# Optimization experiments

Measured on AMD Instinct MI355X. Metric: run time of the kernel, lower is better.

## Reference

```python
import jax, jax.numpy as jnp
import numpy as np

UP = 2
KSIZE = 3
RES = 64
LRELU_SLOPE = 0.2
ACT_GAIN = float(np.sqrt(2.0))  # def_gain of 'lrelu' in bias_act


def _setup_filter():
    # upfirdn2d.setup_filter([1,3,3,1]): normalize, make separable 2D filter
    f = jnp.array([1.0, 3.0, 3.0, 1.0], dtype=jnp.float32)
    f = f / jnp.sum(f)
    return jnp.outer(f, f)  # [4,4]


def _upfirdn2d_up2(x, f2):
    # Zero-insertion upsample by 2 + pad + FIR filter, gain = up**2.
    # Torch path: zero-insert to 2H, pad (3,2), conv 4-tap -> 2H+2.
    # lhs_dilation gives 2H-1; absorbing the trailing inserted zero into the
    # right pad ((3,3) instead of (3,2)) is exactly equivalent.
    B, C, H, W = x.shape
    k = (f2 * (UP * UP)).astype(x.dtype)[None, None]  # [1,1,4,4] (symmetric, flip-invariant)
    k = jnp.tile(k, (C, 1, 1, 1))                     # depthwise [C,1,4,4]
    return jax.lax.conv_general_dilated(
        x, k, window_strides=(1, 1), padding=((3, 3), (3, 3)),
        lhs_dilation=(UP, UP),
        dimension_numbers=('NCHW', 'OIHW', 'NCHW'),
        feature_group_count=C)


def setup_inputs() -> dict:
    key = jax.random.key(0)
    ks = jax.random.split(key, 6)
    B, Cin, Cout, Wd = 16, 512, 512, 512
    Hin = RES // UP
    return {
        "x": jax.random.normal(ks[0], (B, Cin, Hin, Hin), jnp.float32),
        "w": jax.random.normal(ks[1], (B, Wd), jnp.float32),
        "affine_weight": jax.random.normal(ks[2], (Cin, Wd), jnp.float32),
        "affine_bias": jnp.ones((Cin,), jnp.float32),  # bias_init=1
        "weight": jax.random.normal(ks[3], (Cout, Cin, KSIZE, KSIZE), jnp.float32),
        "bias": jnp.zeros((Cout,), jnp.float32),
        "noise_const": jax.random.normal(ks[4], (RES, RES), jnp.float32),
        "noise_strength": jax.random.uniform(ks[5], (), jnp.float32),
    }


def reference(x, w, affine_weight, affine_bias, weight, bias, noise_const, noise_strength):
    B, Cin, Hin, Win = x.shape
    Cout = weight.shape[0]
    # affine: FullyConnectedLayer, weight_gain = 1/sqrt(w_dim), bias_init=1
    styles = w @ affine_weight.T * (1.0 / np.sqrt(w.shape[1])) + affine_bias  # [B,Cin]
    # modulate + demodulate (fused_modconv=True): per-sample weights
    wmod = weight[None] * styles[:, None, :, None, None]                     # [B,Cout,Cin,kh,kw]
    dcoef = jax.lax.rsqrt(jnp.sum(jnp.square(wmod), axis=(2, 3, 4)) + 1e-8)  # [B,Cout]
    wmod = wmod * dcoef[:, :, None, None, None]
    # up=2 -> flip_weight=False -> true convolution: flip spatial taps
    wmod = wmod[..., ::-1, ::-1]
    # conv2d_resample: upfirdn2d upsample first (pad = k//2 + (fw+up-1)//2 = 3), then VALID conv
    xu = _upfirdn2d_up2(x, _setup_filter())                                  # [B,Cin,66,66]
    xr = xu.reshape(1, B * Cin, xu.shape[2], xu.shape[3])
    wr = wmod.reshape(B * Cout, Cin, KSIZE, KSIZE)
    y = jax.lax.conv_general_dilated(
        xr, wr, window_strides=(1, 1), padding='VALID',
        dimension_numbers=('NCHW', 'OIHW', 'NCHW'),
        feature_group_count=B)
    y = y.reshape(B, Cout, RES, RES)
    # noise_mode='const': noise = noise_const * noise_strength
    y = y + noise_const * noise_strength
    # fused bias + lrelu + def_gain (gain=1, conv_clamp=None)
    y = jax.nn.leaky_relu(y + bias[None, :, None, None], LRELU_SLOPE) * ACT_GAIN
    return y
```

## Files before the change

kernel.cpp:

```cpp
#include <hip/hip_runtime.h>
#include <hip/hip_bf16.h>
#include <math.h>

#define CIN   512
#define COUT  512
#define NB    16
#define WD    512
#define HIN   32
#define RES   64
#define LRELU 0.2f
#define ACT_GAIN 1.4142135623730951f

typedef __attribute__((ext_vector_type(8))) short short8;
typedef __attribute__((ext_vector_type(4))) float float4v;
typedef __attribute__((ext_vector_type(16))) float float16v;

__global__ void styles2_kernel(const float* __restrict__ w,
                               const float* __restrict__ aw,
                               const float* __restrict__ ab,
                               float* __restrict__ styles) {
    int b = blockIdx.x;
    int cig = blockIdx.y;
    int lane = threadIdx.x & 63, wv = threadIdx.x >> 6;
    __shared__ float wsh[WD];
    for (int e = threadIdx.x; e < WD; e += 256) wsh[e] = w[b * WD + e];
    __syncthreads();
    for (int r = 0; r < 16; ++r) {
        int ci = cig * 64 + wv * 16 + r;
        const float* arow = aw + (size_t)ci * WD;
        float acc = 0.f;
        for (int k = lane; k < WD; k += 64) acc += arow[k] * wsh[k];
        for (int off = 32; off; off >>= 1) acc += __shfl_down(acc, off, 64);
        if (lane == 0)
            styles[b * CIN + ci] = acc * 0.04419417382415922f + ab[ci];
    }
}

__global__ void prep_weights(const float* __restrict__ weight,
                             float* __restrict__ wsq,
                             __hip_bfloat16* __restrict__ gb) {
    int gid = blockIdx.x * 256 + threadIdx.x;
    int co = gid & 511;
    int cig = gid >> 9;
    int cc = cig >> 2, chi = cig & 3;
    int cib = cc * 32 + chi * 8;
    int cog = co >> 5, colo = co & 31;

    float wv[8][3][3];
#pragma unroll
    for (int clo = 0; clo < 8; ++clo) {
        const float* wp = weight + ((size_t)co * CIN + cib + clo) * 9;
        float s = 0.f;
#pragma unroll
        for (int ay = 0; ay < 3; ++ay)
#pragma unroll
            for (int ax = 0; ax < 3; ++ax) {
                float v = wp[ay * 3 + ax];
                wv[clo][ay][ax] = v;
                s += v * v;
            }
        wsq[(size_t)co * CIN + cib + clo] = s;
    }

    const float cr[2][3][3] = {
        {{0.f, 0.25f, 0.75f}, {0.75f, 0.75f, 0.25f}, {0.25f, 0.f, 0.f}},
        {{0.f, 0.f, 0.25f},  {0.25f, 0.75f, 0.75f}, {0.75f, 0.25f, 0.f}}};

#pragma unroll
    for (int phy = 0; phy < 2; ++phy) {
        float tmp[8][3][3];
#pragma unroll
        for (int clo = 0; clo < 8; ++clo)
#pragma unroll
            for (int dy = 0; dy < 3; ++dy)
#pragma unroll
                for (int ax = 0; ax < 3; ++ax)
                    tmp[clo][dy][ax] = cr[phy][dy][0] * wv[clo][0][ax]
                                     + cr[phy][dy][1] * wv[clo][1][ax]
                                     + cr[phy][dy][2] * wv[clo][2][ax];
#pragma unroll
        for (int phx = 0; phx < 2; ++phx) {
            int n = phx * 32 + colo;
#pragma unroll
            for (int dy = 0; dy < 3; ++dy)
#pragma unroll
                for (int dx = 0; dx < 3; ++dx) {
                    int t = dy * 3 + dx;
                    short8 sv;
#pragma unroll
                    for (int clo = 0; clo < 8; ++clo) {
                        float g = tmp[clo][dy][0] * cr[phx][dx][0]
                                + tmp[clo][dy][1] * cr[phx][dx][1]
                                + tmp[clo][dy][2] * cr[phx][dx][2];
                        __hip_bfloat16 h = __float2bfloat16(g);
                        sv[clo] = *reinterpret_cast<const short*>(&h);
                    }
                    size_t off = ((((((size_t)cc * 2 + phy) * 9 + t) * 4 + chi)
                                   * 16 + cog) * 64 + n) * 8;
                    *reinterpret_cast<short8*>(gb + off) = sv;
                }
        }
    }
}

__global__ void dcoef2_kernel(const float* __restrict__ styles,
                              const float* __restrict__ wsq,
                              float* __restrict__ dcoef) {
    int b = blockIdx.x;
    int cog = blockIdx.y;
    int lane = threadIdx.x & 63, wv = threadIdx.x >> 6;
    __shared__ float s2[CIN];
    for (int e = threadIdx.x; e < CIN; e += 256) {
        float s = styles[b * CIN + e];
        s2[e] = s * s;
    }
    __syncthreads();
    for (int r = 0; r < 16; ++r) {
        int co = cog * 64 + wv * 16 + r;
        const float* qrow = wsq + (size_t)co * CIN;
        float acc = 0.f;
        for (int k = lane; k < CIN; k += 64) acc += qrow[k] * s2[k];
        for (int off = 32; off; off >>= 1) acc += __shfl_down(acc, off, 64);
        if (lane == 0) dcoef[b * COUT + co] = rsqrtf(acc + 1e-8f);
    }
}

__global__ void xmod_kernel(const float* __restrict__ x,
                            const float* __restrict__ styles,
                            __hip_bfloat16* __restrict__ xb) {
    __shared__ float xt[128 * 36];
    __shared__ float ssh[128];
    const int r = blockIdx.x;
    const int ci0 = blockIdx.y * 128;
    const int b = blockIdx.z;
    if (threadIdx.x < 128) ssh[threadIdx.x] = styles[b * CIN + ci0 + threadIdx.x];
    const bool inr = (r >= 1) && (r <= 32);
    if (inr) {
        for (int e = threadIdx.x; e < 1024; e += 256) {
            int ci = e >> 3, iw4 = e & 7;
            float4v v = *(const float4v*)(
                x + ((size_t)(b * CIN + ci0 + ci) * HIN + (r - 1)) * HIN + iw4 * 4);
            *(float4v*)(&xt[ci * 36 + iw4 * 4]) = v;
        }
    }
    __syncthreads();
    for (int e = threadIdx.x; e < 544; e += 256) {
        int c = e >> 4, t16 = e & 15;
        short8 sv;
#pragma unroll
        for (int u = 0; u < 8; ++u) {
            int ci = t16 * 8 + u;
            float val = 0.f;
            if (inr && c >= 1 && c <= 32) val = xt[ci * 36 + (c - 1)] * ssh[ci];
            __hip_bfloat16 h = __float2bfloat16(val);
            sv[u] = *reinterpret_cast<const short*>(&h);
        }
        *reinterpret_cast<short8*>(
            xb + (((size_t)b * 34 + r) * 34 + c) * CIN + ci0 + t16 * 8) = sv;
    }
}

#define ABUF 39936
#define BBUF 36864
#define BUFSZ (ABUF + BBUF)
#define LDS_TOT (2 * BUFSZ)

__global__ __launch_bounds__(512, 1) void conv_mfma(
        const __hip_bfloat16* __restrict__ xb,
        const __hip_bfloat16* __restrict__ gb,
        const float* __restrict__ dcoef,
        const float* __restrict__ bias,
        const float* __restrict__ noise,
        const float* __restrict__ nstr,
        float* __restrict__ out)
{
    extern __shared__ __align__(16) char smem[];
    const int tid = threadIdx.x;
    const int lane = tid & 63;
    const int wid = tid >> 6;
    const int li32 = lane & 31;
    const int hi = lane >> 5;
    const int mb = blockIdx.x;
    const int cog = blockIdx.y;
    const int bz = blockIdx.z;
    const int b  = bz >> 1;
    const int phy = bz & 1;
    const int y0 = mb * 16;

    int a_goff[5];
#pragma unroll
    for (int k = 0; k < 5; ++k) {
        int n = wid + k * 8;
        int s = n * 64 + lane;
        if (s > 2447) s = 2447;
        int cr = s / 136;
        int rem = s - cr * 136;
        int chi = rem / 34;
        int col = rem - chi * 34;
        a_goff[k] = (((b * 34 + y0 + cr) * 34 + col)) * CIN + chi * 8;
    }
    int b_goff[5];
#pragma unroll
    for (int k = 0; k < 5; ++k) {
        int sl = wid + k * 8;
        b_goff[k] = phy * 589824 + (sl * 16 + cog) * 1024 + lane * 16;
    }

    float16v acc[2][2];
#pragma unroll
    for (int i = 0; i < 2; ++i)
#pragma unroll
        for (int j = 0; j < 2; ++j) acc[i][j] = (float16v)0.f;

    const char* xg = (const char*)xb;
    const char* wg = (const char*)gb;

#define STAGE(CC, BUFB) do {                                                  \
        _Pragma("unroll")                                                     \
        for (int k = 0; k < 5; ++k) {                                         \
            int sl = wid + k * 8;                                             \
            if (sl < 36) {                                                    \
                long ge = (long)b_goff[k] + (long)(CC) * 1179648;             \
                __builtin_amdgcn_global_load_lds(                             \
                    (const __attribute__((address_space(1))) char*)(wg + ge), \
                    (__attribute__((address_space(3))) char*)(smem + (BUFB) + ABUF + sl * 1024), \
                    16, 0, 0);                                                \
            }                                                                 \
        }                                                                     \
        _Pragma("unroll")                                                     \
        for (int k = 0; k < 5; ++k) {                                         \
            int n = wid + k * 8;                                              \
            if (n < 39) {                                                     \
                long ge = (long)(a_goff[k] + (CC) * 32);                      \
                __builtin_amdgcn_global_load_lds(                             \
                    (const __attribute__((address_space(1))) char*)(xg + ge * 2), \
                    (__attribute__((address_space(3))) char*)(smem + (BUFB) + n * 1024), \
                    16, 0, 0);                                                \
            }                                                                 \
        }                                                                     \
    } while (0)

#define LOADF(BUFB, S, SLOT) do {                                             \
        const int t_ = (S) >> 1, ks_ = (S) & 1;                               \
        const int dy1 = t_ / 3, dx1 = t_ - dy1 * 3;                           \
        _Pragma("unroll")                                                     \
        for (int nf = 0; nf < 2; ++nf)                                        \
            fB[SLOT][nf] = *(const short8*)(smem + (BUFB) + ABUF +            \
                    (((t_ * 4 + ks_ * 2 + hi) * 64) + nf * 32 + li32) * 16);  \
        _Pragma("unroll")                                                     \
        for (int mf = 0; mf < 2; ++mf)                                        \
            fA[SLOT][mf] = *(const short8*)(smem + (BUFB) +                   \
                    ((((wid * 2 + mf + dy1) * 4 + ks_ * 2 + hi) * 34) +       \
                     (li32 + dx1)) * 16);                                     \
    } while (0)

#define COMPUTE(BUFB) do {                                                    \
        short8 fA[2][2], fB[2][2];                                            \
        LOADF(BUFB, 0, 0);                                                    \
        __builtin_amdgcn_sched_group_barrier(0x100, 4, 0);    \
        __builtin_amdgcn_s_setprio(1);                                        \
        _Pragma("unroll")                                                     \
        for (int s = 0; s < 18; ++s) {                                        \
            const int cur = s & 1, nxt = cur ^ 1;                             \
            if (s < 17) LOADF(BUFB, s + 1, nxt);                              \
            _Pragma("unroll")                                                 \
            for (int mf = 0; mf < 2; ++mf)                                    \
                _Pragma("unroll")                                             \
                for (int nf = 0; nf < 2; ++nf)                                \
                    acc[mf][nf] = __builtin_amdgcn_mfma_f32_32x32x16_bf16(    \
                        fA[cur][mf], fB[cur][nf], acc[mf][nf], 0, 0, 0);      \
            if (s < 17)                                                       \
                __builtin_amdgcn_sched_group_barrier(0x100, 4, 0);  \
            __builtin_amdgcn_sched_group_barrier(0x008, 4, 0);      \
        }                                                                     \
        __builtin_amdgcn_s_setprio(0);                                        \
    } while (0)

#define SYNC() do {                                                           \
        asm volatile("s_waitcnt vmcnt(0)" ::: "memory");                      \
        __builtin_amdgcn_s_barrier();                                         \
    } while (0)

    STAGE(0, 0);
    SYNC();

#pragma unroll 1
    for (int cc = 0; cc < 16; cc += 2) {
        STAGE(cc + 1, BUFSZ);
        COMPUTE(0);
        SYNC();
        if (cc + 2 < 16) STAGE(cc + 2, 0);
        COMPUTE(BUFSZ);
        SYNC();
    }

#undef STAGE
#undef LOADF
#undef COMPUTE
#undef SYNC

    const float ns = nstr[0];
    const int cout = cog * 32 + li32;
    const float dc = dcoef[b * COUT + cout];
    const float bs = bias[cout];
#pragma unroll
    for (int mf = 0; mf < 2; ++mf) {
        int ic = y0 + wid * 2 + mf;
        int fr = 2 * ic + phy;
        float* op = out + ((size_t)(b * COUT + cout) * RES + fr) * RES;
        const float* npz = noise + fr * RES;
#pragma unroll
        for (int r2 = 0; r2 < 4; ++r2) {
            int fcb = 16 * r2 + 8 * hi;
            float nzv[8];
            *(float4v*)&nzv[0] = *(const float4v*)(npz + fcb);
            *(float4v*)&nzv[4] = *(const float4v*)(npz + fcb + 4);
            float f[8];
#pragma unroll
            for (int uu = 0; uu < 4; ++uu) {
#pragma unroll
                for (int nf = 0; nf < 2; ++nf) {
                    float v = acc[mf][nf][r2 * 4 + uu] * dc
                            + nzv[2 * uu + nf] * ns + bs;
                    f[2 * uu + nf] = (v > 0.f ? v : LRELU * v) * ACT_GAIN;
                }
            }
            *(float4v*)(op + fcb)     = *(const float4v*)&f[0];
            *(float4v*)(op + fcb + 4) = *(const float4v*)&f[4];
        }
    }
}

extern "C" void kernel_launch(void* const* d_in, const int* in_sizes, int n_in,
                              void* d_out, int out_size, void* d_ws, size_t ws_size,
                              hipStream_t stream) {
    (void)in_sizes; (void)n_in; (void)out_size; (void)ws_size;
    const float* x     = (const float*)d_in[0];
    const float* w     = (const float*)d_in[1];
    const float* aw    = (const float*)d_in[2];
    const float* ab    = (const float*)d_in[3];
    const float* wt    = (const float*)d_in[4];
    const float* bias  = (const float*)d_in[5];
    const float* noise = (const float*)d_in[6];
    const float* nstr  = (const float*)d_in[7];
    float* out = (float*)d_out;

    static bool init = false;
    if (!init) {
        hipFuncSetAttribute(reinterpret_cast<const void*>(conv_mfma),
                            hipFuncAttributeMaxDynamicSharedMemorySize, LDS_TOT);
        init = true;
    }

    char* ws = (char*)d_ws;
    float* styles = (float*)ws;
    float* dcoef  = (float*)(ws + 32768);
    float* wsq    = (float*)(ws + 65536);
    __hip_bfloat16* gb = (__hip_bfloat16*)(ws + 65536 + 1048576);
    __hip_bfloat16* xb = (__hip_bfloat16*)(ws + 65536 + 1048576 + 18874368);

    styles2_kernel<<<dim3(NB, 8), dim3(256), 0, stream>>>(w, aw, ab, styles);
    prep_weights<<<dim3(128), dim3(256), 0, stream>>>(wt, wsq, gb);
    dcoef2_kernel<<<dim3(NB, 8), dim3(256), 0, stream>>>(styles, wsq, dcoef);
    xmod_kernel<<<dim3(34, 4, NB), dim3(256), 0, stream>>>(x, styles, xb);
    conv_mfma<<<dim3(2, 16, NB * 2), dim3(512), LDS_TOT, stream>>>(
        xb, gb, dcoef, bias, noise, nstr, out);
}
```

Baseline: 494.7 us.

## Double output-channel tile per block and halve K-chunk to reuse A tiles

Each conv block now computes 64 output channels (two 32-channel groups) instead of 32, halving the grid's y dimension, while the per-stage input-channel chunk is halved (16 instead of 32) so the A tile in LDS shrinks and the loop runs 32 stages. Each A fragment now feeds four MFMAs instead of two, reducing redundant global loads of the upsampled activations across blocks. The change costs more accumulator registers (8 float16 vectors), twice as many barrier-synchronised stages and fewer blocks to fill the GPU.

New measurement: 488.0 us. Within noise of the previous version (-1.4%).

```diff
diff --git a/kernel.cpp b/kernel.cpp
--- a/kernel.cpp
+++ b/kernel.cpp
@@ -160,7 +160,7 @@
     }
 }
 
-#define ABUF 39936
+#define ABUF 20480
 #define BBUF 36864
 #define BUFSZ (ABUF + BBUF)
 #define LDS_TOT (2 * BUFSZ)
@@ -181,36 +181,38 @@
     const int li32 = lane & 31;
     const int hi = lane >> 5;
     const int mb = blockIdx.x;
-    const int cog = blockIdx.y;
+    const int cogp = blockIdx.y;
     const int bz = blockIdx.z;
     const int b  = bz >> 1;
     const int phy = bz & 1;
     const int y0 = mb * 16;
 
-    int a_goff[5];
-#pragma unroll
-    for (int k = 0; k < 5; ++k) {
+    int a_goff[3];
+#pragma unroll
+    for (int k = 0; k < 3; ++k) {
         int n = wid + k * 8;
         int s = n * 64 + lane;
-        if (s > 2447) s = 2447;
-        int cr = s / 136;
-        int rem = s - cr * 136;
-        int chi = rem / 34;
-        int col = rem - chi * 34;
-        a_goff[k] = (((b * 34 + y0 + cr) * 34 + col)) * CIN + chi * 8;
+        if (s > 1223) s = 1223;
+        int cr = s / 68;
+        int rem = s - cr * 68;
+        int kh = rem / 34;
+        int col = rem - kh * 34;
+        a_goff[k] = ((b * 34 + y0 + cr) * 34 + col) * 512 + kh * 8;
     }
     int b_goff[5];
 #pragma unroll
     for (int k = 0; k < 5; ++k) {
         int sl = wid + k * 8;
-        b_goff[k] = phy * 589824 + (sl * 16 + cog) * 1024 + lane * 16;
-    }
-
-    float16v acc[2][2];
+        int t = sl >> 2, g = (sl >> 1) & 1, kh = sl & 1;
+        b_goff[k] = (phy * 9 + t) * 65536 + kh * 16384
+                  + (cogp * 2 + g) * 1024 + lane * 16;
+    }
+
+    float16v acc[2][4];
 #pragma unroll
     for (int i = 0; i < 2; ++i)
 #pragma unroll
-        for (int j = 0; j < 2; ++j) acc[i][j] = (float16v)0.f;
+        for (int j = 0; j < 4; ++j) acc[i][j] = (float16v)0.f;
 
     const char* xg = (const char*)xb;
     const char* wg = (const char*)gb;
@@ -220,7 +222,8 @@
         for (int k = 0; k < 5; ++k) {                                         \
             int sl = wid + k * 8;                                             \
             if (sl < 36) {                                                    \
-                long ge = (long)b_goff[k] + (long)(CC) * 1179648;             \
+                long ge = (long)b_goff[k] + (long)((CC) >> 1) * 1179648       \
+                        + (long)((CC) & 1) * 32768;                           \
                 __builtin_amdgcn_global_load_lds(                             \
                     (const __attribute__((address_space(1))) char*)(wg + ge), \
                     (__attribute__((address_space(3))) char*)(smem + (BUFB) + ABUF + sl * 1024), \
@@ -228,10 +231,10 @@
             }                                                                 \
         }                                                                     \
         _Pragma("unroll")                                                     \
-        for (int k = 0; k < 5; ++k) {                                         \
+        for (int k = 0; k < 3; ++k) {                                         \
             int n = wid + k * 8;                                              \
-            if (n < 39) {                                                     \
-                long ge = (long)(a_goff[k] + (CC) * 32);                      \
+            if (n < 20) {                                                     \
+                long ge = (long)(a_goff[k] + (CC) * 16);                      \
                 __builtin_amdgcn_global_load_lds(                             \
                     (const __attribute__((address_space(1))) char*)(xg + ge * 2), \
                     (__attribute__((address_space(3))) char*)(smem + (BUFB) + n * 1024), \
@@ -240,38 +243,38 @@
         }                                                                     \
     } while (0)
 
-#define LOADF(BUFB, S, SLOT) do {                                             \
-        const int t_ = (S) >> 1, ks_ = (S) & 1;                               \
-        const int dy1 = t_ / 3, dx1 = t_ - dy1 * 3;                           \
-        _Pragma("unroll")                                                     \
-        for (int nf = 0; nf < 2; ++nf)                                        \
+#define LOADF(BUFB, T, SLOT) do {                                             \
+        const int dy_ = (T) / 3, dx_ = (T) - dy_ * 3;                         \
+        _Pragma("unroll")                                                     \
+        for (int nf = 0; nf < 4; ++nf) {                                      \
+            const int g_ = nf >> 1, px_ = nf & 1;                             \
             fB[SLOT][nf] = *(const short8*)(smem + (BUFB) + ABUF +            \
-                    (((t_ * 4 + ks_ * 2 + hi) * 64) + nf * 32 + li32) * 16);  \
+                    ((((T) * 2 + g_) * 2 + hi) * 64 + px_ * 32 + li32) * 16); \
+        }                                                                     \
         _Pragma("unroll")                                                     \
         for (int mf = 0; mf < 2; ++mf)                                        \
             fA[SLOT][mf] = *(const short8*)(smem + (BUFB) +                   \
-                    ((((wid * 2 + mf + dy1) * 4 + ks_ * 2 + hi) * 34) +       \
-                     (li32 + dx1)) * 16);                                     \
+                    (((wid * 2 + mf + dy_) * 2 + hi) * 34 + li32 + dx_) * 16);\
     } while (0)
 
 #define COMPUTE(BUFB) do {                                                    \
-        short8 fA[2][2], fB[2][2];                                            \
+        short8 fA[2][2], fB[2][4];                                            \
         LOADF(BUFB, 0, 0);                                                    \
-        __builtin_amdgcn_sched_group_barrier(0x100, 4, 0);    \
+        __builtin_amdgcn_sched_group_barrier(0x100, 6, 0);     \
         __builtin_amdgcn_s_setprio(1);                                        \
         _Pragma("unroll")                                                     \
-        for (int s = 0; s < 18; ++s) {                                        \
+        for (int s = 0; s < 9; ++s) {                                         \
             const int cur = s & 1, nxt = cur ^ 1;                             \
-            if (s < 17) LOADF(BUFB, s + 1, nxt);                              \
+            if (s < 8) LOADF(BUFB, s + 1, nxt);                               \
             _Pragma("unroll")                                                 \
             for (int mf = 0; mf < 2; ++mf)                                    \
                 _Pragma("unroll")                                             \
-                for (int nf = 0; nf < 2; ++nf)                                \
+                for (int nf = 0; nf < 4; ++nf)                                \
                     acc[mf][nf] = __builtin_amdgcn_mfma_f32_32x32x16_bf16(    \
                         fA[cur][mf], fB[cur][nf], acc[mf][nf], 0, 0, 0);      \
-            if (s < 17)                                                       \
-                __builtin_amdgcn_sched_group_barrier(0x100, 4, 0);  \
-            __builtin_amdgcn_sched_group_barrier(0x008, 4, 0);      \
+            if (s < 8)                                                        \
+                __builtin_amdgcn_sched_group_barrier(0x100, 6, 0);   \
+            __builtin_amdgcn_sched_group_barrier(0x008, 8, 0);     \
         }                                                                     \
         __builtin_amdgcn_s_setprio(0);                                        \
     } while (0)
@@ -285,11 +288,11 @@
     SYNC();
 
 #pragma unroll 1
-    for (int cc = 0; cc < 16; cc += 2) {
+    for (int cc = 0; cc < 32; cc += 2) {
         STAGE(cc + 1, BUFSZ);
         COMPUTE(0);
         SYNC();
-        if (cc + 2 < 16) STAGE(cc + 2, 0);
+        if (cc + 2 < 32) STAGE(cc + 2, 0);
         COMPUTE(BUFSZ);
         SYNC();
     }
@@ -300,33 +303,36 @@
 #undef SYNC
 
     const float ns = nstr[0];
-    const int cout = cog * 32 + li32;
-    const float dc = dcoef[b * COUT + cout];
-    const float bs = bias[cout];
-#pragma unroll
-    for (int mf = 0; mf < 2; ++mf) {
-        int ic = y0 + wid * 2 + mf;
-        int fr = 2 * ic + phy;
-        float* op = out + ((size_t)(b * COUT + cout) * RES + fr) * RES;
-        const float* npz = noise + fr * RES;
-#pragma unroll
-        for (int r2 = 0; r2 < 4; ++r2) {
-            int fcb = 16 * r2 + 8 * hi;
-            float nzv[8];
-            *(float4v*)&nzv[0] = *(const float4v*)(npz + fcb);
-            *(float4v*)&nzv[4] = *(const float4v*)(npz + fcb + 4);
-            float f[8];
-#pragma unroll
-            for (int uu = 0; uu < 4; ++uu) {
-#pragma unroll
-                for (int nf = 0; nf < 2; ++nf) {
-                    float v = acc[mf][nf][r2 * 4 + uu] * dc
-                            + nzv[2 * uu + nf] * ns + bs;
-                    f[2 * uu + nf] = (v > 0.f ? v : LRELU * v) * ACT_GAIN;
+#pragma unroll
+    for (int g = 0; g < 2; ++g) {
+        int cout = (cogp * 2 + g) * 32 + li32;
+        float dc = dcoef[b * COUT + cout];
+        float bs = bias[cout];
+#pragma unroll
+        for (int mf = 0; mf < 2; ++mf) {
+            int ic = y0 + wid * 2 + mf;
+            int fr = 2 * ic + phy;
+            float* op = out + ((size_t)(b * COUT + cout) * RES + fr) * RES;
+            const float* npz = noise + fr * RES;
+#pragma unroll
+            for (int r2 = 0; r2 < 4; ++r2) {
+                int fcb = 16 * r2 + 8 * hi;
+                float nzv[8];
+                *(float4v*)&nzv[0] = *(const float4v*)(npz + fcb);
+                *(float4v*)&nzv[4] = *(const float4v*)(npz + fcb + 4);
+                float f[8];
+#pragma unroll
+                for (int uu = 0; uu < 4; ++uu) {
+#pragma unroll
+                    for (int px = 0; px < 2; ++px) {
+                        float v = acc[mf][g * 2 + px][r2 * 4 + uu] * dc
+                                + nzv[2 * uu + px] * ns + bs;
+                        f[2 * uu + px] = (v > 0.f ? v : LRELU * v) * ACT_GAIN;
+                    }
                 }
+                *(float4v*)(op + fcb)     = *(const float4v*)&f[0];
+                *(float4v*)(op + fcb + 4) = *(const float4v*)&f[4];
             }
-            *(float4v*)(op + fcb)     = *(const float4v*)&f[0];
-            *(float4v*)(op + fcb + 4) = *(const float4v*)&f[4];
         }
     }
 }
@@ -363,6 +369,6 @@
     prep_weights<<<dim3(128), dim3(256), 0, stream>>>(wt, wsq, gb);
     dcoef2_kernel<<<dim3(NB, 8), dim3(256), 0, stream>>>(styles, wsq, dcoef);
     xmod_kernel<<<dim3(34, 4, NB), dim3(256), 0, stream>>>(x, styles, xb);
-    conv_mfma<<<dim3(2, 16, NB * 2), dim3(512), LDS_TOT, stream>>>(
+    conv_mfma<<<dim3(2, 8, NB * 2), dim3(512), LDS_TOT, stream>>>(
         xb, gb, dcoef, bias, noise, nstr, out);
 }
```
